# Optimization experiments

Measured on AMD Instinct MI355X. Metric: run time of the kernel, lower is better.

The kernel has to match this reference:

```python
import jax, jax.numpy as jnp
import numpy as np

N = 50000
E = 800000
IN_C = 256
OUT_C = 256
HEADS = 8
HEAD_C = OUT_C // HEADS  # 32
BNECK = OUT_C // 4       # 64
NEG_SLOPE = 0.2
BN_EPS = 1e-5


def _bn(x, gamma, beta):
    # BatchNorm1d over node dim, batch statistics (deterministic train-mode math)
    mu = jnp.mean(x, axis=0)
    var = jnp.var(x, axis=0)
    return (x - mu) * jax.lax.rsqrt(var + BN_EPS) * gamma + beta


def setup_inputs() -> dict:
    key = jax.random.key(0)
    ks = jax.random.split(key, 16)
    s = lambda fan: 1.0 / np.sqrt(fan)
    x = jax.random.normal(ks[0], (N, IN_C), dtype=jnp.float32)
    edge_index = jax.random.randint(ks[1], (2, E), 0, N, dtype=jnp.int64)
    return {
        "x": x,
        "edge_index": edge_index,
        # GATConv params (lin has no bias in PyG)
        "W_lin": jax.random.normal(ks[2], (IN_C, HEADS * HEAD_C), jnp.float32) * s(IN_C),
        "att_src": jax.random.normal(ks[3], (HEADS, HEAD_C), jnp.float32) * s(HEAD_C),
        "att_dst": jax.random.normal(ks[4], (HEADS, HEAD_C), jnp.float32) * s(HEAD_C),
        "conv_bias": jnp.zeros((HEADS * HEAD_C,), jnp.float32),
        "W_res": jax.random.normal(ks[5], (IN_C, HEADS * HEAD_C), jnp.float32) * s(IN_C),
        # gnn.BatchNorm
        "g_norm": jnp.ones((OUT_C,), jnp.float32),
        "b_norm": jnp.zeros((OUT_C,), jnp.float32),
        # Bottleneck down
        "W_down": jax.random.normal(ks[6], (OUT_C, BNECK), jnp.float32) * s(OUT_C),
        "b_down": jnp.zeros((BNECK,), jnp.float32),
        "g_down": jnp.ones((BNECK,), jnp.float32),
        "bb_down": jnp.zeros((BNECK,), jnp.float32),
        # Bottleneck up
        "W_up": jax.random.normal(ks[7], (BNECK, OUT_C), jnp.float32) * s(BNECK),
        "b_up": jnp.zeros((OUT_C,), jnp.float32),
        "g_up": jnp.ones((OUT_C,), jnp.float32),
        "bb_up": jnp.zeros((OUT_C,), jnp.float32),
    }


def _forward(x, edge_index, W_lin, att_src, att_dst, conv_bias, W_res,
             g_norm, b_norm, W_down, b_down, g_down, bb_down,
             W_up, b_up, g_up, bb_up):
    src, dst = edge_index[0], edge_index[1]
    # --- GATConv ---
    xh = (x @ W_lin).reshape(N, HEADS, HEAD_C)            # [N,H,C]
    a_src = jnp.einsum("nhc,hc->nh", xh, att_src)          # [N,H]
    a_dst = jnp.einsum("nhc,hc->nh", xh, att_dst)          # [N,H]
    e = a_src[src] + a_dst[dst]                             # [E,H]
    e = jnp.where(e > 0, e, NEG_SLOPE * e)                  # leaky_relu
    # segment softmax over destination nodes (numerically stable)
    m = jax.ops.segment_max(e, dst, num_segments=N)         # [N,H]
    m = jnp.where(jnp.isfinite(m), m, 0.0)
    ex = jnp.exp(e - m[dst])
    denom = jax.ops.segment_sum(ex, dst, num_segments=N)    # [N,H]
    alpha = ex / (denom[dst] + 1e-16)                        # [E,H]
    msgs = xh[src] * alpha[:, :, None]                       # [E,H,C]
    out = jax.ops.segment_sum(msgs, dst, num_segments=N)    # [N,H,C]
    out = out.reshape(N, HEADS * HEAD_C) + conv_bias + x @ W_res  # GAT residual + bias
    # --- norm + act ---
    h = jax.nn.elu(_bn(out, g_norm, b_norm))
    # --- bottleneck ---
    d = jax.nn.elu(_bn(h @ W_down + b_down, g_down, bb_down))
    u = jax.nn.elu(_bn(d @ W_up + b_up, g_up, bb_up))
    h = h + u
    # dropout: eval mode (identity); in==out so identity skip
    return h + x


def reference(x, edge_index, W_lin, att_src, att_dst, conv_bias, W_res,
              g_norm, b_norm, W_down, b_down, g_down, bb_down,
              W_up, b_up, g_up, bb_up):
    return _forward(x, edge_index, W_lin, att_src, att_dst, conv_bias, W_res,
                    g_norm, b_norm, W_down, b_down, g_down, bb_down,
                    W_up, b_up, g_up, bb_up)
```

## Files before the change

kernel.cpp:

```cpp
#include <hip/hip_runtime.h>

#define NN 50000
#define EE 800000
#define HEADS 8
#define NEG 0.2f
#define BN_EPS 1e-5f
#define SCAN_B 196

typedef unsigned int uint;
typedef unsigned short ushort;

typedef __bf16 bf16x8 __attribute__((ext_vector_type(8)));
typedef float f32x4 __attribute__((ext_vector_type(4)));

__device__ __forceinline__ float bflo(uint u) { return __uint_as_float(u << 16); }
__device__ __forceinline__ float bfhi(uint u) { return __uint_as_float(u & 0xffff0000u); }
__device__ __forceinline__ float bf1(ushort u) { return __uint_as_float(((uint)u) << 16); }
__device__ __forceinline__ ushort f2bf(float f) {
  uint u = __float_as_uint(f);
  u += 0x7fff + ((u >> 16) & 1);
  return (ushort)(u >> 16);
}
__device__ __forceinline__ float eluf(float v) { return v > 0.f ? v : expm1f(v); }

__global__ void k_detect(const uint* __restrict__ xw, const int* __restrict__ ew,
                         int* __restrict__ flags) {
  if (threadIdx.x == 0 && blockIdx.x == 0) {
    int good = 0;
    for (int i = 0; i < 256; ++i) {
      uint lo = xw[i] & 0xffffu;
      uint ex = (lo >> 7) & 0xffu;
      if (ex >= 110u && ex <= 140u) good++;
    }
    flags[0] = (good >= 128) ? 1 : 0;
    int zeros = 0;
    for (int i = 0; i < 256; ++i)
      if (ew[2 * i + 1] == 0) zeros++;
    flags[1] = (zeros >= 200) ? 1 : 0;
  }
}

__global__ void k_params(const void* p0, const void* p1, const void* p2, const void* p3,
                         const void* p4, const void* p5, const void* p6, const void* p7,
                         const void* p8, const void* p9, const void* p10,
                         float* __restrict__ P, const int* __restrict__ flags) {
  const void* srcs[11] = {p0, p1, p2, p3, p4, p5, p6, p7, p8, p9, p10};
  const int sz[11]  = {256, 256, 256, 256, 256, 64, 64, 64, 256, 256, 256};
  const int off[11] = {0, 256, 512, 768, 1024, 1280, 1344, 1408, 1472, 1728, 1984};
  int b = blockIdx.x, t = threadIdx.x;
  if (t < sz[b]) {
    const void* s = srcs[b];
    float v = flags[0] ? bf1(((const ushort*)s)[t]) : ((const float*)s)[t];
    P[off[b] + t] = v;
  }
}

__global__ void k_transpose(const void* __restrict__ src, ushort* __restrict__ dst,
                            int R, int C, const int* __restrict__ flags) {
  int c = blockIdx.x;
  if (c >= C) {
    for (int r = threadIdx.x; r < R; r += blockDim.x) dst[(size_t)c * R + r] = 0;
    return;
  }
  int bf = flags[0];
  for (int r = threadIdx.x; r < R; r += blockDim.x) {
    float v = bf ? bf1(((const ushort*)src)[(size_t)r * C + c])
                 : ((const float*)src)[(size_t)r * C + c];
    dst[(size_t)c * R + r] = f2bf(v);
  }
}

__global__ void k_cast(const void* __restrict__ x, ushort* __restrict__ xb,
                       const int* __restrict__ flags) {
  size_t base = ((size_t)blockIdx.x * 256 + threadIdx.x) * 8;
  if (base >= (size_t)NN * 256) return;
  if (flags[0]) {
    *(uint4*)(xb + base) = *(const uint4*)((const ushort*)x + base);
  } else {
    const float* xf = (const float*)x;
    float4 a = *(const float4*)(xf + base);
    float4 b = *(const float4*)(xf + base + 4);
    uint4 o;
    o.x = (uint)f2bf(a.x) | ((uint)f2bf(a.y) << 16);
    o.y = (uint)f2bf(a.z) | ((uint)f2bf(a.w) << 16);
    o.z = (uint)f2bf(b.x) | ((uint)f2bf(b.y) << 16);
    o.w = (uint)f2bf(b.z) | ((uint)f2bf(b.w) << 16);
    *(uint4*)(xb + base) = o;
  }
}

__global__ void k_edges(const int* __restrict__ raw, int* __restrict__ sc, int* __restrict__ dc,
                        int* __restrict__ count, const int* __restrict__ flags) {
  int e = blockIdx.x * 256 + threadIdx.x;
  if (e >= EE) return;
  int s, d;
  if (flags[1]) { s = raw[2 * e]; d = raw[2 * (EE + e)]; }
  else          { s = raw[e];     d = raw[EE + e]; }
  if ((uint)s >= NN) s = 0;
  if ((uint)d >= NN) d = 0;
  sc[e] = s; dc[e] = d;
  atomicAdd(&count[d], 1);
}

__global__ __launch_bounds__(256)
void k_gemm(const ushort* __restrict__ A, const ushort* __restrict__ Bt,
            int M, int K, int mode,
            ushort* __restrict__ o_xh, ushort* __restrict__ o_xres,
            float* __restrict__ o_f32, int NC, const float* __restrict__ bias) {
  __shared__ __align__(16) ushort As[128 * 32];
  __shared__ __align__(16) ushort Bs[128 * 32];
  int t = threadIdx.x;
  int l = t & 63, w = t >> 6;
  int wr = w >> 1, wc = w & 1;
  int lr = l & 15, lq = l >> 4;
  int m0 = blockIdx.x * 128;
  int n0 = blockIdx.y * 128;

  f32x4 acc[4][4];
#pragma unroll
  for (int i = 0; i < 4; ++i)
#pragma unroll
    for (int j = 0; j < 4; ++j) acc[i][j] = (f32x4){0.f, 0.f, 0.f, 0.f};

  for (int kt = 0; kt < K; kt += 32) {
    __syncthreads();
#pragma unroll
    for (int r = 0; r < 2; ++r) {
      int ci = r * 256 + t;
      int m = ci >> 2, ko = (ci & 3) << 3;
      int gm = m0 + m; gm = gm < M ? gm : M - 1;
      *(uint4*)(&As[m * 32 + ko]) = *(const uint4*)(A + (size_t)gm * K + kt + ko);
      *(uint4*)(&Bs[m * 32 + ko]) = *(const uint4*)(Bt + (size_t)(n0 + m) * K + kt + ko);
    }
    __syncthreads();
    bf16x8 af[4], bf[4];
#pragma unroll
    for (int i = 0; i < 4; ++i) {
      af[i] = *(const bf16x8*)(&As[(wr * 64 + i * 16 + lr) * 32 + lq * 8]);
      bf[i] = *(const bf16x8*)(&Bs[(wc * 64 + i * 16 + lr) * 32 + lq * 8]);
    }
#pragma unroll
    for (int i = 0; i < 4; ++i)
#pragma unroll
      for (int j = 0; j < 4; ++j)
        acc[i][j] = __builtin_amdgcn_mfma_f32_16x16x32_bf16(af[i], bf[j], acc[i][j], 0, 0, 0);
  }

#pragma unroll
  for (int i = 0; i < 4; ++i) {
    int gr0 = m0 + wr * 64 + i * 16 + lq * 4;
#pragma unroll
    for (int j = 0; j < 4; ++j) {
      int gc = n0 + wc * 64 + j * 16 + lr;
#pragma unroll
      for (int r = 0; r < 4; ++r) {
        int row = gr0 + r;
        if (row >= M) continue;
        float v = acc[i][j][r];
        if (mode == 0) {
          if (gc < 256) o_xh[(size_t)row * 256 + gc] = f2bf(v);
          else          o_xres[(size_t)row * 256 + (gc - 256)] = f2bf(v);
        } else {
          if (gc < NC) o_f32[(size_t)row * NC + gc] = v + bias[gc];
        }
      }
    }
  }
}

__global__ void k_attn(const ushort* __restrict__ xh, const float* __restrict__ P,
                       float* __restrict__ a_src, float* __restrict__ a_dst) {
  int id = blockIdx.x * 256 + threadIdx.x;
  if (id >= NN * HEADS) return;
  int n = id >> 3, h = id & 7;
  const uint4* xr = (const uint4*)(xh + (size_t)n * 256 + h * 32);
  const float4* pa = (const float4*)(P + h * 32);
  const float4* pd = (const float4*)(P + 256 + h * 32);
  float s = 0.f, d = 0.f;
#pragma unroll
  for (int j = 0; j < 4; ++j) {
    uint4 q = xr[j];
    float4 a0 = pa[2 * j], a1 = pa[2 * j + 1];
    float4 d0 = pd[2 * j], d1 = pd[2 * j + 1];
    float x0 = bflo(q.x), x1 = bfhi(q.x), x2 = bflo(q.y), x3 = bfhi(q.y);
    float x4 = bflo(q.z), x5 = bfhi(q.z), x6 = bflo(q.w), x7 = bfhi(q.w);
    s += x0 * a0.x + x1 * a0.y + x2 * a0.z + x3 * a0.w
       + x4 * a1.x + x5 * a1.y + x6 * a1.z + x7 * a1.w;
    d += x0 * d0.x + x1 * d0.y + x2 * d0.z + x3 * d0.w
       + x4 * d1.x + x5 * d1.y + x6 * d1.z + x7 * d1.w;
  }
  a_src[id] = s; a_dst[id] = d;
}

__global__ void k_scan_bs(const int* __restrict__ count, int* __restrict__ bsum) {
  __shared__ int s[256];
  int i = blockIdx.x * 256 + threadIdx.x;
  s[threadIdx.x] = (i < NN) ? count[i] : 0;
  __syncthreads();
  for (int off = 128; off > 0; off >>= 1) {
    if (threadIdx.x < off) s[threadIdx.x] += s[threadIdx.x + off];
    __syncthreads();
  }
  if (threadIdx.x == 0) bsum[blockIdx.x] = s[0];
}

__global__ void k_scan_top(const int* __restrict__ bsum, int* __restrict__ boff,
                           int* __restrict__ rowptr) {
  __shared__ int s[256];
  int t = threadIdx.x;
  int v = (t < SCAN_B) ? bsum[t] : 0;
  s[t] = v;
  __syncthreads();
  for (int off = 1; off < 256; off <<= 1) {
    int u = (t >= off) ? s[t - off] : 0;
    __syncthreads();
    s[t] += u;
    __syncthreads();
  }
  boff[t] = s[t] - v;
  if (t == 255) rowptr[NN] = s[255];
}

__global__ void k_scan_wr(const int* __restrict__ count, const int* __restrict__ boff,
                          int* __restrict__ rowptr, int* __restrict__ rowwork) {
  __shared__ int s[256];
  int b = blockIdx.x, t = threadIdx.x;
  int i = b * 256 + t;
  int v = (i < NN) ? count[i] : 0;
  s[t] = v;
  __syncthreads();
  for (int off = 1; off < 256; off <<= 1) {
    int u = (t >= off) ? s[t - off] : 0;
    __syncthreads();
    s[t] += u;
    __syncthreads();
  }
  if (i < NN) {
    int ex = boff[b] + s[t] - v;
    rowptr[i] = ex;
    rowwork[i] = ex;
  }
}

__global__ void k_scatter(const int* __restrict__ sc, const int* __restrict__ dc,
                          int* __restrict__ rowwork, int* __restrict__ perm_src) {
  int e = blockIdx.x * 256 + threadIdx.x;
  if (e >= EE) return;
  int pos = atomicAdd(&rowwork[dc[e]], 1);
  perm_src[pos] = sc[e];
}

__global__ __launch_bounds__(256)
void k_aggregate(const int* __restrict__ rowptr, const int* __restrict__ perm_src,
                 const float* __restrict__ a_src, const float* __restrict__ a_dst,
                 const ushort* __restrict__ xh, const ushort* __restrict__ xres,
                 const float* __restrict__ bias, float* __restrict__ out) {
  int n = blockIdx.x * 4 + (threadIdx.x >> 6);
  int l = threadIdx.x & 63;
  if (n >= NN) return;
  int h = l >> 3;
  float ad = a_dst[n * 8 + h];
  int st = rowptr[n], en = rowptr[n + 1];
  float a0 = 0.f, a1 = 0.f, a2 = 0.f, a3 = 0.f, sum = 0.f;
  for (int p = st; p < en; ++p) {
    int s = perm_src[p];
    float v = a_src[s * 8 + h] + ad;
    v = v > 0.f ? v : NEG * v;
    v = fminf(v, 60.f);
    float wgt = __expf(v);
    sum += wgt;
    uint2 q = *(const uint2*)(xh + (size_t)s * 256 + l * 4);
    a0 += wgt * bflo(q.x);
    a1 += wgt * bfhi(q.x);
    a2 += wgt * bflo(q.y);
    a3 += wgt * bfhi(q.y);
  }
  float inv = 1.0f / (sum + 1e-16f);
  int cb = l * 4;
  float4 qb = *(const float4*)(bias + cb);
  uint2 qr = *(const uint2*)(xres + (size_t)n * 256 + cb);
  float4 o;
  o.x = a0 * inv + qb.x + bflo(qr.x);
  o.y = a1 * inv + qb.y + bfhi(qr.x);
  o.z = a2 * inv + qb.z + bflo(qr.y);
  o.w = a3 * inv + qb.w + bfhi(qr.y);
  *(float4*)(out + (size_t)n * 256 + cb) = o;
}

__global__ void k_stats(const float* __restrict__ x, float* __restrict__ sums, int n, int C) {
  int t = threadIdx.x;
  int c = t & (C - 1);
  int rl = t / C;
  int rpb = 256 / C;
  int rows = (n + gridDim.x - 1) / gridDim.x;
  int r0 = blockIdx.x * rows;
  int r1 = r0 + rows; if (r1 > n) r1 = n;
  float s = 0.f, ss = 0.f;
  for (int r = r0 + rl; r < r1; r += rpb) {
    float v = x[(size_t)r * C + c];
    s += v; ss += v * v;
  }
  atomicAdd(&sums[c], s);
  atomicAdd(&sums[C + c], ss);
}

__global__ void k_bnact1(const float* __restrict__ xin, const float* __restrict__ sums,
                         const float* __restrict__ g, const float* __restrict__ b,
                         ushort* __restrict__ h1b) {
  int id = blockIdx.x * 256 + threadIdx.x;
  size_t base = (size_t)id * 4;
  if (base >= (size_t)NN * 256) return;
  int c = (int)(base & 255);
  const float invN = 1.0f / NN;
  float4 sm = *(const float4*)(sums + c);
  float4 sq = *(const float4*)(sums + 256 + c);
  float4 g4 = *(const float4*)(g + c);
  float4 b4 = *(const float4*)(b + c);
  float4 v = *(const float4*)(xin + base);
  float vv[4] = {v.x, v.y, v.z, v.w};
  float smv[4] = {sm.x, sm.y, sm.z, sm.w}, sqv[4] = {sq.x, sq.y, sq.z, sq.w};
  float gv[4] = {g4.x, g4.y, g4.z, g4.w}, bv[4] = {b4.x, b4.y, b4.z, b4.w};
  float o[4];
#pragma unroll
  for (int j = 0; j < 4; ++j) {
    float mean = smv[j] * invN;
    float var = sqv[j] * invN - mean * mean;
    float sc = gv[j] * rsqrtf(var + BN_EPS);
    o[j] = eluf((vv[j] - mean) * sc + bv[j]);
  }
  uint2 pk;
  pk.x = (uint)f2bf(o[0]) | ((uint)f2bf(o[1]) << 16);
  pk.y = (uint)f2bf(o[2]) | ((uint)f2bf(o[3]) << 16);
  *(uint2*)(h1b + base) = pk;
}

__global__ void k_bnact2(const float* __restrict__ xin, const float* __restrict__ sums,
                         const float* __restrict__ g, const float* __restrict__ b,
                         ushort* __restrict__ db) {
  int id = blockIdx.x * 256 + threadIdx.x;
  size_t base = (size_t)id * 4;
  if (base >= (size_t)NN * 64) return;
  int c = (int)(base & 63);
  const float invN = 1.0f / NN;
  float4 sm = *(const float4*)(sums + c);
  float4 sq = *(const float4*)(sums + 64 + c);
  float4 g4 = *(const float4*)(g + c);
  float4 b4 = *(const float4*)(b + c);
  float4 v = *(const float4*)(xin + base);
  float vv[4] = {v.x, v.y, v.z, v.w};
  float smv[4] = {sm.x, sm.y, sm.z, sm.w}, sqv[4] = {sq.x, sq.y, sq.z, sq.w};
  float gv[4] = {g4.x, g4.y, g4.z, g4.w}, bv[4] = {b4.x, b4.y, b4.z, b4.w};
  float o[4];
#pragma unroll
  for (int j = 0; j < 4; ++j) {
    float mean = smv[j] * invN;
    float var = sqv[j] * invN - mean * mean;
    float sc = gv[j] * rsqrtf(var + BN_EPS);
    o[j] = eluf((vv[j] - mean) * sc + bv[j]);
  }
  uint2 pk;
  pk.x = (uint)f2bf(o[0]) | ((uint)f2bf(o[1]) << 16);
  pk.y = (uint)f2bf(o[2]) | ((uint)f2bf(o[3]) << 16);
  *(uint2*)(db + base) = pk;
}

__global__ void k_final(const float* __restrict__ upre, const float* __restrict__ sums,
                        const float* __restrict__ g, const float* __restrict__ b,
                        const ushort* __restrict__ h1b, const void* __restrict__ xsrc,
                        void* __restrict__ outv, const int* __restrict__ flags) {
  int id = blockIdx.x * 256 + threadIdx.x;
  size_t base = (size_t)id * 4;
  if (base >= (size_t)NN * 256) return;
  int c = (int)(base & 255);
  const float invN = 1.0f / NN;
  float4 sm = *(const float4*)(sums + c);
  float4 sq = *(const float4*)(sums + 256 + c);
  float4 g4 = *(const float4*)(g + c);
  float4 b4 = *(const float4*)(b + c);
  float4 v = *(const float4*)(upre + base);
  uint2 qh = *(const uint2*)(h1b + base);
  float xv[4];
  if (flags[0]) {
    uint2 qx = *(const uint2*)((const ushort*)xsrc + base);
    xv[0] = bflo(qx.x); xv[1] = bfhi(qx.x); xv[2] = bflo(qx.y); xv[3] = bfhi(qx.y);
  } else {
    float4 qx = *(const float4*)((const float*)xsrc + base);
    xv[0] = qx.x; xv[1] = qx.y; xv[2] = qx.z; xv[3] = qx.w;
  }
  float vv[4] = {v.x, v.y, v.z, v.w};
  float hv[4] = {bflo(qh.x), bfhi(qh.x), bflo(qh.y), bfhi(qh.y)};
  float smv[4] = {sm.x, sm.y, sm.z, sm.w}, sqv[4] = {sq.x, sq.y, sq.z, sq.w};
  float gv[4] = {g4.x, g4.y, g4.z, g4.w}, bv[4] = {b4.x, b4.y, b4.z, b4.w};
  float o[4];
#pragma unroll
  for (int j = 0; j < 4; ++j) {
    float mean = smv[j] * invN;
    float var = sqv[j] * invN - mean * mean;
    float sc = gv[j] * rsqrtf(var + BN_EPS);
    o[j] = eluf((vv[j] - mean) * sc + bv[j]) + hv[j] + xv[j];
  }
  if (flags[0]) {
    uint2 pk;
    pk.x = (uint)f2bf(o[0]) | ((uint)f2bf(o[1]) << 16);
    pk.y = (uint)f2bf(o[2]) | ((uint)f2bf(o[3]) << 16);
    *(uint2*)((ushort*)outv + base) = pk;
  } else {
    *(float4*)((float*)outv + base) = make_float4(o[0], o[1], o[2], o[3]);
  }
}

extern "C" void kernel_launch(void* const* d_in, const int* in_sizes, int n_in,
                              void* d_out, int out_size, void* d_ws, size_t ws_size,
                              hipStream_t stream) {
  const void* x      = d_in[0];
  const int*  ei     = (const int*)d_in[1];
  const void* W_lin  = d_in[2];
  const void* att_s  = d_in[3];
  const void* att_d  = d_in[4];
  const void* c_bias = d_in[5];
  const void* W_res  = d_in[6];
  const void* g_norm = d_in[7];
  const void* b_norm = d_in[8];
  const void* W_down = d_in[9];
  const void* b_down = d_in[10];
  const void* g_down = d_in[11];
  const void* bb_down= d_in[12];
  const void* W_up   = d_in[13];
  const void* b_up   = d_in[14];
  const void* g_up   = d_in[15];
  const void* bb_up  = d_in[16];

  char* ws = (char*)d_ws;
  size_t off = 0;
  auto alloc = [&](size_t bytes) -> char* {
    char* p = ws + off;
    off = (off + bytes + 255) & ~(size_t)255;
    return p;
  };
  int*   flags  = (int*)alloc(2 * 4);
  int*   count  = (int*)alloc((size_t)NN * 4);
  float* sums1  = (float*)alloc(512 * 4);
  float* sums2  = (float*)alloc(128 * 4);
  float* sums3  = (float*)alloc(512 * 4);
  size_t zbytes = off;
  float* P      = (float*)alloc(2240 * 4);
  int* bsum     = (int*)alloc(256 * 4);
  int* boff     = (int*)alloc(256 * 4);
  int* rowptr   = (int*)alloc((size_t)(NN + 1) * 4);
  int* rowwork  = (int*)alloc((size_t)(NN + 1) * 4);
  int* src_c    = (int*)alloc((size_t)EE * 4);
  int* dst_c    = (int*)alloc((size_t)EE * 4);
  int* perm_src = (int*)alloc((size_t)EE * 4);
  ushort* bt1   = (ushort*)alloc((size_t)512 * 256 * 2);
  ushort* bt2   = (ushort*)alloc((size_t)128 * 256 * 2);
  ushort* bt3   = (ushort*)alloc((size_t)256 * 64 * 2);
  float* a_src  = (float*)alloc((size_t)NN * 8 * 4);
  float* a_dst  = (float*)alloc((size_t)NN * 8 * 4);
  ushort* x_bf  = (ushort*)alloc((size_t)NN * 256 * 2);
  ushort* xh    = (ushort*)alloc((size_t)NN * 256 * 2);
  ushort* xres  = (ushort*)alloc((size_t)NN * 256 * 2);
  float* out_gat= (float*)alloc((size_t)NN * 256 * 4);
  ushort* d_b   = (ushort*)alloc((size_t)NN * 64 * 2);
  ushort* h1b  = x_bf;
  float*  d_pre = (float*)xres;
  float*  u_pre = out_gat;

  hipMemsetAsync(d_ws, 0, zbytes, stream);

  hipLaunchKernelGGL(k_detect, dim3(1), dim3(64), 0, stream, (const uint*)x, ei, flags);
  hipLaunchKernelGGL(k_params, dim3(11), dim3(256), 0, stream,
                     att_s, att_d, c_bias, g_norm, b_norm, b_down, g_down, bb_down,
                     b_up, g_up, bb_up, P, flags);
  hipLaunchKernelGGL(k_transpose, dim3(256), dim3(256), 0, stream, W_lin, bt1, 256, 256, flags);
  hipLaunchKernelGGL(k_transpose, dim3(256), dim3(256), 0, stream, W_res, bt1 + 256 * 256, 256, 256, flags);
  hipLaunchKernelGGL(k_transpose, dim3(128), dim3(256), 0, stream, W_down, bt2, 256, 64, flags);
  hipLaunchKernelGGL(k_transpose, dim3(256), dim3(64),  0, stream, W_up, bt3, 64, 256, flags);
  hipLaunchKernelGGL(k_cast, dim3(6250), dim3(256), 0, stream, x, x_bf, flags);
  hipLaunchKernelGGL(k_edges, dim3((EE + 255) / 256), dim3(256), 0, stream,
                     ei, src_c, dst_c, count, flags);

  hipLaunchKernelGGL(k_gemm, dim3(391, 4), dim3(256), 0, stream, x_bf, bt1, NN, 256, 0,
                     xh, xres, (float*)nullptr, 0, (const float*)nullptr);
  hipLaunchKernelGGL(k_attn, dim3((NN * 8 + 255) / 256), dim3(256), 0, stream,
                     xh, P, a_src, a_dst);

  hipLaunchKernelGGL(k_scan_bs, dim3(SCAN_B), dim3(256), 0, stream, count, bsum);
  hipLaunchKernelGGL(k_scan_top, dim3(1), dim3(256), 0, stream, bsum, boff, rowptr);
  hipLaunchKernelGGL(k_scan_wr, dim3(SCAN_B), dim3(256), 0, stream, count, boff, rowptr, rowwork);
  hipLaunchKernelGGL(k_scatter, dim3((EE + 255) / 256), dim3(256), 0, stream,
                     src_c, dst_c, rowwork, perm_src);

  hipLaunchKernelGGL(k_aggregate, dim3(NN / 4), dim3(256), 0, stream, rowptr, perm_src,
                     a_src, a_dst, xh, xres, P + 512, out_gat);

  hipLaunchKernelGGL(k_stats, dim3(256), dim3(256), 0, stream, out_gat, sums1, NN, 256);
  hipLaunchKernelGGL(k_bnact1, dim3(NN * 256 / 4 / 256), dim3(256), 0, stream,
                     out_gat, sums1, P + 768, P + 1024, h1b);

  hipLaunchKernelGGL(k_gemm, dim3(391, 1), dim3(256), 0, stream, h1b, bt2, NN, 256, 1,
                     (ushort*)nullptr, (ushort*)nullptr, d_pre, 64, P + 1280);
  hipLaunchKernelGGL(k_stats, dim3(256), dim3(256), 0, stream, d_pre, sums2, NN, 64);
  hipLaunchKernelGGL(k_bnact2, dim3(NN * 64 / 4 / 256), dim3(256), 0, stream,
                     d_pre, sums2, P + 1344, P + 1408, d_b);

  hipLaunchKernelGGL(k_gemm, dim3(391, 2), dim3(256), 0, stream, d_b, bt3, NN, 64, 2,
                     (ushort*)nullptr, (ushort*)nullptr, u_pre, 256, P + 1472);
  hipLaunchKernelGGL(k_stats, dim3(256), dim3(256), 0, stream, u_pre, sums3, NN, 256);
  hipLaunchKernelGGL(k_final, dim3(NN * 256 / 4 / 256), dim3(256), 0, stream,
                     u_pre, sums3, P + 1728, P + 1984, h1b, x, d_out, flags);
}
```

Baseline: 648.5 us.

## Parallelize detect, tile weight transpose, swap GEMM grid order, widen aggregate loads

Several independent changes. The flag-detection kernel now uses a 64-lane wave reduction instead of a single thread. Weight transposes go through a 64x64 shared-memory tile for coalesced reads and writes. GEMM grids are swapped so consecutive blocks share the same A row tile, which improves L2 reuse. The edge aggregation splits each node's edges across two half-waves using 16-byte loads and combines them with a cross-half shuffle, cutting per-edge serial iterations at the cost of more registers.

```diff
diff --git a/kernel.cpp b/kernel.cpp
--- a/kernel.cpp
+++ b/kernel.cpp
@@ -25,19 +25,17 @@
 
 __global__ void k_detect(const uint* __restrict__ xw, const int* __restrict__ ew,
                          int* __restrict__ flags) {
-  if (threadIdx.x == 0 && blockIdx.x == 0) {
-    int good = 0;
-    for (int i = 0; i < 256; ++i) {
-      uint lo = xw[i] & 0xffffu;
-      uint ex = (lo >> 7) & 0xffu;
-      if (ex >= 110u && ex <= 140u) good++;
-    }
-    flags[0] = (good >= 128) ? 1 : 0;
-    int zeros = 0;
-    for (int i = 0; i < 256; ++i)
-      if (ew[2 * i + 1] == 0) zeros++;
-    flags[1] = (zeros >= 200) ? 1 : 0;
-  }
+  int l = threadIdx.x;
+  int good = 0, zeros = 0;
+#pragma unroll
+  for (int j = 0; j < 4; ++j) {
+    uint lo = xw[l * 4 + j] & 0xffffu;
+    uint ex = (lo >> 7) & 0xffu;
+    good += (ex >= 110u && ex <= 140u) ? 1 : 0;
+    zeros += (ew[2 * (l * 4 + j) + 1] == 0) ? 1 : 0;
+  }
+  for (int o = 32; o; o >>= 1) { good += __shfl_down(good, o); zeros += __shfl_down(zeros, o); }
+  if (l == 0) { flags[0] = (good >= 128) ? 1 : 0; flags[1] = (zeros >= 200) ? 1 : 0; }
 }
 
 __global__ void k_params(const void* p0, const void* p1, const void* p2, const void* p3,
@@ -56,17 +54,31 @@
 }
 
 __global__ void k_transpose(const void* __restrict__ src, ushort* __restrict__ dst,
-                            int R, int C, const int* __restrict__ flags) {
-  int c = blockIdx.x;
-  if (c >= C) {
-    for (int r = threadIdx.x; r < R; r += blockDim.x) dst[(size_t)c * R + r] = 0;
-    return;
-  }
+                            int R, int C, int D, const int* __restrict__ flags) {
+  __shared__ ushort tile[64][65];
+  int r0 = blockIdx.x * 64, c0 = blockIdx.y * 64;
+  int t = threadIdx.x;
+  int tr = t >> 6;
+  int tc = t & 63;
   int bf = flags[0];
-  for (int r = threadIdx.x; r < R; r += blockDim.x) {
-    float v = bf ? bf1(((const ushort*)src)[(size_t)r * C + c])
-                 : ((const float*)src)[(size_t)r * C + c];
-    dst[(size_t)c * R + r] = f2bf(v);
+#pragma unroll
+  for (int i = 0; i < 16; ++i) {
+    int rl = tr + i * 4;
+    int r = r0 + rl, c = c0 + tc;
+    float v = 0.f;
+    if (r < R && c < C)
+      v = bf ? bf1(((const ushort*)src)[(size_t)r * C + c])
+             : ((const float*)src)[(size_t)r * C + c];
+    tile[rl][tc] = f2bf(v);
+  }
+  __syncthreads();
+#pragma unroll
+  for (int i = 0; i < 16; ++i) {
+    int cl = tr + i * 4;
+    int rl = tc;
+    int c = c0 + cl, r = r0 + rl;
+    if (c < D && r < R)
+      dst[(size_t)c * R + r] = (c < C) ? tile[rl][cl] : (ushort)0;
   }
 }
 
@@ -113,8 +125,8 @@
   int l = t & 63, w = t >> 6;
   int wr = w >> 1, wc = w & 1;
   int lr = l & 15, lq = l >> 4;
-  int m0 = blockIdx.x * 128;
-  int n0 = blockIdx.y * 128;
+  int m0 = blockIdx.y * 128;
+  int n0 = blockIdx.x * 128;
 
   f32x4 acc[4][4];
 #pragma unroll
@@ -258,33 +270,49 @@
   int n = blockIdx.x * 4 + (threadIdx.x >> 6);
   int l = threadIdx.x & 63;
   if (n >= NN) return;
-  int h = l >> 3;
+  int half = l >> 5;
+  int q = l & 31;
+  int h = q >> 2;
   float ad = a_dst[n * 8 + h];
   int st = rowptr[n], en = rowptr[n + 1];
-  float a0 = 0.f, a1 = 0.f, a2 = 0.f, a3 = 0.f, sum = 0.f;
-  for (int p = st; p < en; ++p) {
+  float a0 = 0.f, a1 = 0.f, a2 = 0.f, a3 = 0.f;
+  float a4 = 0.f, a5 = 0.f, a6 = 0.f, a7 = 0.f, sum = 0.f;
+#pragma unroll 2
+  for (int p = st + half; p < en; p += 2) {
     int s = perm_src[p];
     float v = a_src[s * 8 + h] + ad;
     v = v > 0.f ? v : NEG * v;
-    v = fminf(v, 60.f);
-    float wgt = __expf(v);
+    float wgt = __expf(fminf(v, 60.f));
     sum += wgt;
-    uint2 q = *(const uint2*)(xh + (size_t)s * 256 + l * 4);
-    a0 += wgt * bflo(q.x);
-    a1 += wgt * bfhi(q.x);
-    a2 += wgt * bflo(q.y);
-    a3 += wgt * bfhi(q.y);
-  }
-  float inv = 1.0f / (sum + 1e-16f);
-  int cb = l * 4;
-  float4 qb = *(const float4*)(bias + cb);
-  uint2 qr = *(const uint2*)(xres + (size_t)n * 256 + cb);
-  float4 o;
-  o.x = a0 * inv + qb.x + bflo(qr.x);
-  o.y = a1 * inv + qb.y + bfhi(qr.x);
-  o.z = a2 * inv + qb.z + bflo(qr.y);
-  o.w = a3 * inv + qb.w + bfhi(qr.y);
-  *(float4*)(out + (size_t)n * 256 + cb) = o;
+    uint4 t4 = *(const uint4*)(xh + (size_t)s * 256 + q * 8);
+    a0 += wgt * bflo(t4.x); a1 += wgt * bfhi(t4.x);
+    a2 += wgt * bflo(t4.y); a3 += wgt * bfhi(t4.y);
+    a4 += wgt * bflo(t4.z); a5 += wgt * bfhi(t4.z);
+    a6 += wgt * bflo(t4.w); a7 += wgt * bfhi(t4.w);
+  }
+  sum += __shfl_xor(sum, 32);
+  a0 += __shfl_xor(a0, 32); a1 += __shfl_xor(a1, 32);
+  a2 += __shfl_xor(a2, 32); a3 += __shfl_xor(a3, 32);
+  a4 += __shfl_xor(a4, 32); a5 += __shfl_xor(a5, 32);
+  a6 += __shfl_xor(a6, 32); a7 += __shfl_xor(a7, 32);
+  if (half == 0) {
+    float inv = 1.0f / (sum + 1e-16f);
+    int cb = q * 8;
+    float4 b0 = *(const float4*)(bias + cb);
+    float4 b1 = *(const float4*)(bias + cb + 4);
+    uint4 qr = *(const uint4*)(xres + (size_t)n * 256 + cb);
+    float4 o0, o1;
+    o0.x = a0 * inv + b0.x + bflo(qr.x);
+    o0.y = a1 * inv + b0.y + bfhi(qr.x);
+    o0.z = a2 * inv + b0.z + bflo(qr.y);
+    o0.w = a3 * inv + b0.w + bfhi(qr.y);
+    o1.x = a4 * inv + b1.x + bflo(qr.z);
+    o1.y = a5 * inv + b1.y + bfhi(qr.z);
+    o1.z = a6 * inv + b1.z + bflo(qr.w);
+    o1.w = a7 * inv + b1.w + bfhi(qr.w);
+    *(float4*)(out + (size_t)n * 256 + cb) = o0;
+    *(float4*)(out + (size_t)n * 256 + cb + 4) = o1;
+  }
 }
 
 __global__ void k_stats(const float* __restrict__ x, float* __restrict__ sums, int n, int C) {
@@ -471,15 +499,15 @@
   hipLaunchKernelGGL(k_params, dim3(11), dim3(256), 0, stream,
                      att_s, att_d, c_bias, g_norm, b_norm, b_down, g_down, bb_down,
                      b_up, g_up, bb_up, P, flags);
-  hipLaunchKernelGGL(k_transpose, dim3(256), dim3(256), 0, stream, W_lin, bt1, 256, 256, flags);
-  hipLaunchKernelGGL(k_transpose, dim3(256), dim3(256), 0, stream, W_res, bt1 + 256 * 256, 256, 256, flags);
-  hipLaunchKernelGGL(k_transpose, dim3(128), dim3(256), 0, stream, W_down, bt2, 256, 64, flags);
-  hipLaunchKernelGGL(k_transpose, dim3(256), dim3(64),  0, stream, W_up, bt3, 64, 256, flags);
+  hipLaunchKernelGGL(k_transpose, dim3(4, 4), dim3(256), 0, stream, W_lin, bt1, 256, 256, 256, flags);
+  hipLaunchKernelGGL(k_transpose, dim3(4, 4), dim3(256), 0, stream, W_res, bt1 + 256 * 256, 256, 256, 256, flags);
+  hipLaunchKernelGGL(k_transpose, dim3(4, 2), dim3(256), 0, stream, W_down, bt2, 256, 64, 128, flags);
+  hipLaunchKernelGGL(k_transpose, dim3(1, 4), dim3(256), 0, stream, W_up, bt3, 64, 256, 256, flags);
   hipLaunchKernelGGL(k_cast, dim3(6250), dim3(256), 0, stream, x, x_bf, flags);
   hipLaunchKernelGGL(k_edges, dim3((EE + 255) / 256), dim3(256), 0, stream,
                      ei, src_c, dst_c, count, flags);
 
-  hipLaunchKernelGGL(k_gemm, dim3(391, 4), dim3(256), 0, stream, x_bf, bt1, NN, 256, 0,
+  hipLaunchKernelGGL(k_gemm, dim3(4, 391), dim3(256), 0, stream, x_bf, bt1, NN, 256, 0,
                      xh, xres, (float*)nullptr, 0, (const float*)nullptr);
   hipLaunchKernelGGL(k_attn, dim3((NN * 8 + 255) / 256), dim3(256), 0, stream,
                      xh, P, a_src, a_dst);
@@ -497,13 +525,13 @@
   hipLaunchKernelGGL(k_bnact1, dim3(NN * 256 / 4 / 256), dim3(256), 0, stream,
                      out_gat, sums1, P + 768, P + 1024, h1b);
 
-  hipLaunchKernelGGL(k_gemm, dim3(391, 1), dim3(256), 0, stream, h1b, bt2, NN, 256, 1,
+  hipLaunchKernelGGL(k_gemm, dim3(1, 391), dim3(256), 0, stream, h1b, bt2, NN, 256, 1,
                      (ushort*)nullptr, (ushort*)nullptr, d_pre, 64, P + 1280);
   hipLaunchKernelGGL(k_stats, dim3(256), dim3(256), 0, stream, d_pre, sums2, NN, 64);
   hipLaunchKernelGGL(k_bnact2, dim3(NN * 64 / 4 / 256), dim3(256), 0, stream,
                      d_pre, sums2, P + 1344, P + 1408, d_b);
 
-  hipLaunchKernelGGL(k_gemm, dim3(391, 2), dim3(256), 0, stream, d_b, bt3, NN, 64, 2,
+  hipLaunchKernelGGL(k_gemm, dim3(2, 391), dim3(256), 0, stream, d_b, bt3, NN, 64, 2,
                      (ushort*)nullptr, (ushort*)nullptr, u_pre, 256, P + 1472);
   hipLaunchKernelGGL(k_stats, dim3(256), dim3(256), 0, stream, u_pre, sums3, NN, 256);
   hipLaunchKernelGGL(k_final, dim3(NN * 256 / 4 / 256), dim3(256), 0, stream,
```

Result: faster. 613.8 us (-5.3%).
